# Kernel tuning notes

Hardware: AMD Instinct MI355X
Metric: run time of the kernel (lower is better)

Reference implementation:

```python
import jax, jax.numpy as jnp
import numpy as np

H = 1024
V = 50257
S = 4096


def gru_cell(x, h, W_ih, W_hh, b_ih, b_hh):
    # x: (1, in), h: (1, H). PyTorch gate order: r, z, n
    gi = x @ W_ih.T + b_ih  # (1, 3H)
    gh = h @ W_hh.T + b_hh
    i_r, i_z, i_n = jnp.split(gi, 3, axis=1)
    h_r, h_z, h_n = jnp.split(gh, 3, axis=1)
    r = jax.nn.sigmoid(i_r + h_r)
    z = jax.nn.sigmoid(i_z + h_z)
    n = jnp.tanh(i_n + r * h_n)
    return (1.0 - z) * n + z * h


def setup_inputs() -> dict:
    key = jax.random.key(0)
    ks = jax.random.split(key, 16)
    s = 0.02
    return {
        "word_input": jax.random.randint(ks[0], (1,), 0, V),
        "last_context": jax.random.normal(ks[1], (1, H), jnp.float32),
        "last_hidden": jax.random.normal(ks[2], (2, 1, H), jnp.float32),
        "encoder_outputs": jax.random.normal(ks[3], (S, 1, H), jnp.float32),
        "emb": jax.random.normal(ks[4], (V, H), jnp.float32) * s,
        "W_ih0": jax.random.normal(ks[5], (3 * H, 2 * H), jnp.float32) * s,
        "W_hh0": jax.random.normal(ks[6], (3 * H, H), jnp.float32) * s,
        "b_ih0": jnp.zeros((3 * H,), jnp.float32),
        "b_hh0": jnp.zeros((3 * H,), jnp.float32),
        "W_ih1": jax.random.normal(ks[7], (3 * H, H), jnp.float32) * s,
        "W_hh1": jax.random.normal(ks[8], (3 * H, H), jnp.float32) * s,
        "b_ih1": jnp.zeros((3 * H,), jnp.float32),
        "b_hh1": jnp.zeros((3 * H,), jnp.float32),
        "W_attn": jax.random.normal(ks[9], (H, H), jnp.float32) * s,
        "b_attn": jnp.zeros((H,), jnp.float32),
        "W_out": jax.random.normal(ks[10], (V, 2 * H), jnp.float32) * s,
        "b_out": jnp.zeros((V,), jnp.float32),
    }


def reference(word_input, last_context, last_hidden, encoder_outputs,
              emb, W_ih0, W_hh0, b_ih0, b_hh0, W_ih1, W_hh1, b_ih1, b_hh1,
              W_attn, b_attn, W_out, b_out):
    # embedding lookup -> (1, H); rnn input (1, 2H)
    word_embedded = emb[word_input].reshape(1, H)
    rnn_in = jnp.concatenate([word_embedded, last_context], axis=1)
    # 2-layer GRU, single timestep (dropout inactive at eval)
    h0 = gru_cell(rnn_in, last_hidden[0], W_ih0, W_hh0, b_ih0, b_hh0)
    h1 = gru_cell(h0, last_hidden[1], W_ih1, W_hh1, b_ih1, b_hh1)
    rnn_output = h1  # (1, H)
    hidden = jnp.stack([h0, h1], axis=0)  # (2, 1, H)
    # Bahdanau-style attention, batched (replaces per-timestep Python loop)
    enc = encoder_outputs[:, 0, :]  # (S, H)
    energies = (enc @ W_attn.T + b_attn) @ rnn_output[0]  # (S,)
    attn = jax.nn.softmax(energies)  # (S,)
    attn_weights = attn.reshape(1, 1, S)
    context = (attn[None, :] @ enc)  # (1, H)
    # output projection + log-softmax over vocab
    logits = jnp.concatenate([rnn_output, context], axis=1) @ W_out.T + b_out
    output = jax.nn.log_softmax(logits, axis=1)  # (1, V)
    return output, context, hidden, attn_weights
```

## Files before the change

### kernel.cpp

```cpp
#include <hip/hip_runtime.h>
#include <math.h>

constexpr int kH  = 1024;
constexpr int kV  = 50257;
constexpr int kS  = 4096;
constexpr int kH4 = kH / 4;
constexpr int kH2 = 2 * kH;

constexpr int WS_H0     = 0;
constexpr int WS_GH1    = 1024;
constexpr int WS_H1     = 4096;
constexpr int WS_V      = 5120;
constexpr int WS_CTX    = 6144;
constexpr int WS_ATTN   = 7168;
constexpr int WS_E      = 11264;
constexpr int WS_SC     = 15360;
constexpr int WS_PM     = 15424;
constexpr int WS_PS     = 15488;
constexpr int WS_LOGITS = 15552;

constexpr int OUT_LOGITS = 0;
constexpr int OUT_CTX    = kV;
constexpr int OUT_HID    = kV + kH;
constexpr int OUT_ATTN   = kV + kH + 2 * kH;

__device__ __forceinline__ float wred_sum(float v) {
#pragma unroll
  for (int o = 32; o > 0; o >>= 1) v += __shfl_down(v, o, 64);
  return v;
}
__device__ __forceinline__ float wred_max(float v) {
#pragma unroll
  for (int o = 32; o > 0; o >>= 1) v = fmaxf(v, __shfl_down(v, o, 64));
  return v;
}
__device__ __forceinline__ float sigmoidf_(float x) { return 1.0f / (1.0f + __expf(-x)); }
__device__ __forceinline__ float dot4(float4 a, float4 b) {
  return a.x * b.x + a.y * b.y + a.z * b.z + a.w * b.w;
}

__global__ void k1_gru0_gh1(const int* __restrict__ wi_p, const float* __restrict__ lc,
                            const float* __restrict__ lh, const float* __restrict__ emb,
                            const float* __restrict__ W_ih0, const float* __restrict__ W_hh0,
                            const float* __restrict__ b_ih0, const float* __restrict__ b_hh0,
                            const float* __restrict__ W_hh1, const float* __restrict__ b_hh1,
                            float* __restrict__ ws) {
  const int wave = threadIdx.x >> 6, lane = threadIdx.x & 63;
  const int b = blockIdx.x;
  if (b < 256) {
    const int j = b * 4 + wave;
    const int wi = wi_p[0];
    const float4* embr = (const float4*)(emb + (size_t)wi * kH);
    const float4* lc4  = (const float4*)lc;
    const float4* Wr = (const float4*)(W_ih0 + (size_t)j * kH2);
    const float4* Wz = (const float4*)(W_ih0 + (size_t)(j + kH) * kH2);
    const float4* Wn = (const float4*)(W_ih0 + (size_t)(j + 2 * kH) * kH2);
    float ar = 0.f, az = 0.f, an = 0.f;
#pragma unroll
    for (int i = 0; i < 8; i++) {
      const int idx = lane + i * 64;
      const float4 xv = (idx < kH4) ? embr[idx] : lc4[idx - kH4];
      ar += dot4(Wr[idx], xv);
      az += dot4(Wz[idx], xv);
      an += dot4(Wn[idx], xv);
    }
    const float4* Ur = (const float4*)(W_hh0 + (size_t)j * kH);
    const float4* Uz = (const float4*)(W_hh0 + (size_t)(j + kH) * kH);
    const float4* Un = (const float4*)(W_hh0 + (size_t)(j + 2 * kH) * kH);
    const float4* h4 = (const float4*)lh;
    float br = 0.f, bz = 0.f, bn = 0.f;
#pragma unroll
    for (int i = 0; i < 4; i++) {
      const int idx = lane + i * 64;
      const float4 hv = h4[idx];
      br += dot4(Ur[idx], hv);
      bz += dot4(Uz[idx], hv);
      bn += dot4(Un[idx], hv);
    }
    ar = wred_sum(ar); az = wred_sum(az); an = wred_sum(an);
    br = wred_sum(br); bz = wred_sum(bz); bn = wred_sum(bn);
    if (lane == 0) {
      const float ir = ar + b_ih0[j],          hr = br + b_hh0[j];
      const float iz = az + b_ih0[j + kH],     hz = bz + b_hh0[j + kH];
      const float in_ = an + b_ih0[j + 2 * kH], hn = bn + b_hh0[j + 2 * kH];
      const float r = sigmoidf_(ir + hr);
      const float z = sigmoidf_(iz + hz);
      const float n = tanhf(in_ + r * hn);
      ws[WS_H0 + j] = (1.f - z) * n + z * lh[j];
    }
  } else {
    const int row = (b - 256) * 4 + wave;
    const float4* W  = (const float4*)(W_hh1 + (size_t)row * kH);
    const float4* h4 = (const float4*)(lh + kH);
    float a = 0.f;
#pragma unroll
    for (int i = 0; i < 4; i++) {
      const int idx = lane + i * 64;
      a += dot4(W[idx], h4[idx]);
    }
    a = wred_sum(a);
    if (lane == 0) ws[WS_GH1 + row] = a + b_hh1[row];
  }
}

__global__ void k2_gru1(const float* __restrict__ lh, const float* __restrict__ W_ih1,
                        const float* __restrict__ b_ih1, float* __restrict__ ws,
                        float* __restrict__ out) {
  const int wave = threadIdx.x >> 6, lane = threadIdx.x & 63;
  const int j = blockIdx.x * 4 + wave;
  const float4* x4 = (const float4*)(ws + WS_H0);
  const float4* Wr = (const float4*)(W_ih1 + (size_t)j * kH);
  const float4* Wz = (const float4*)(W_ih1 + (size_t)(j + kH) * kH);
  const float4* Wn = (const float4*)(W_ih1 + (size_t)(j + 2 * kH) * kH);
  float ar = 0.f, az = 0.f, an = 0.f;
#pragma unroll
  for (int i = 0; i < 4; i++) {
    const int idx = lane + i * 64;
    const float4 xv = x4[idx];
    ar += dot4(Wr[idx], xv);
    az += dot4(Wz[idx], xv);
    an += dot4(Wn[idx], xv);
  }
  ar = wred_sum(ar); az = wred_sum(az); an = wred_sum(an);
  if (lane == 0) {
    const float r = sigmoidf_(ar + b_ih1[j] + ws[WS_GH1 + j]);
    const float z = sigmoidf_(az + b_ih1[j + kH] + ws[WS_GH1 + j + kH]);
    const float n = tanhf(an + b_ih1[j + 2 * kH] + r * ws[WS_GH1 + j + 2 * kH]);
    const float h1 = (1.f - z) * n + z * lh[kH + j];
    ws[WS_H1 + j] = h1;
    out[OUT_HID + kH + j] = h1;
    out[OUT_HID + j] = ws[WS_H0 + j];
  }
  if (blockIdx.x < 4) ws[WS_V + blockIdx.x * 256 + threadIdx.x] = 0.f;
}

__global__ void k3_attnv(const float* __restrict__ W_attn, const float* __restrict__ b_attn,
                         float* __restrict__ ws) {
  __shared__ float red[4];
  const int b = blockIdx.x, t = threadIdx.x;
  const int wave = t >> 6, lane = t & 63;
  if (b < 64) {
    const float4* W4 = (const float4*)W_attn;
    float4 acc = make_float4(0.f, 0.f, 0.f, 0.f);
    const int j0 = b * 16;
#pragma unroll
    for (int jj = 0; jj < 16; jj++) {
      const int j = j0 + jj;
      const float s = ws[WS_H1 + j];
      const float4 w = W4[(size_t)j * kH4 + t];
      acc.x += s * w.x; acc.y += s * w.y; acc.z += s * w.z; acc.w += s * w.w;
    }
    atomicAdd(&ws[WS_V + 4 * t + 0], acc.x);
    atomicAdd(&ws[WS_V + 4 * t + 1], acc.y);
    atomicAdd(&ws[WS_V + 4 * t + 2], acc.z);
    atomicAdd(&ws[WS_V + 4 * t + 3], acc.w);
  } else {
    float a = 0.f;
    for (int i = t; i < kH; i += 256) a += b_attn[i] * ws[WS_H1 + i];
    const float wsum = wred_sum(a);
    if (lane == 0) red[wave] = wsum;
    __syncthreads();
    if (t == 0) ws[WS_SC + 0] = red[0] + red[1] + red[2] + red[3];
  }
}

__global__ void k4_energies(const float* __restrict__ enc, float* __restrict__ ws) {
  const int wave = threadIdx.x >> 6, lane = threadIdx.x & 63;
  const int s = blockIdx.x * 4 + wave;
  const float4* e4 = (const float4*)(enc + (size_t)s * kH);
  const float4* v4 = (const float4*)(ws + WS_V);
  float a = 0.f;
#pragma unroll
  for (int i = 0; i < 4; i++) {
    const int idx = lane + i * 64;
    a += dot4(e4[idx], v4[idx]);
  }
  a = wred_sum(a);
  if (lane == 0) ws[WS_E + s] = a + ws[WS_SC + 0];
}

__global__ void k5_softmax(float* __restrict__ ws, float* __restrict__ out) {
  __shared__ float red[16];
  const int t = threadIdx.x, lane = t & 63, wave = t >> 6;
  const float4 e = ((const float4*)(ws + WS_E))[t];
  float m = fmaxf(fmaxf(e.x, e.y), fmaxf(e.z, e.w));
  float wm = wred_max(m);
  if (lane == 0) red[wave] = wm;
  __syncthreads();
  if (wave == 0) {
    float x = (lane < 16) ? red[lane] : -INFINITY;
    x = wred_max(x);
    if (lane == 0) red[0] = x;
  }
  __syncthreads();
  m = red[0];
  __syncthreads();
  float4 ex;
  ex.x = __expf(e.x - m); ex.y = __expf(e.y - m);
  ex.z = __expf(e.z - m); ex.w = __expf(e.w - m);
  float s = ex.x + ex.y + ex.z + ex.w;
  float wsum = wred_sum(s);
  if (lane == 0) red[wave] = wsum;
  __syncthreads();
  if (wave == 0) {
    float x = (lane < 16) ? red[lane] : 0.f;
    x = wred_sum(x);
    if (lane == 0) red[0] = x;
  }
  __syncthreads();
  const float inv = 1.0f / red[0];
  float4 a4 = make_float4(ex.x * inv, ex.y * inv, ex.z * inv, ex.w * inv);
  ((float4*)(ws + WS_ATTN))[t] = a4;
  out[OUT_ATTN + 4 * t + 0] = a4.x;
  out[OUT_ATTN + 4 * t + 1] = a4.y;
  out[OUT_ATTN + 4 * t + 2] = a4.z;
  out[OUT_ATTN + 4 * t + 3] = a4.w;
  ws[WS_CTX + t] = 0.f;
}

__global__ void k6_context(const float* __restrict__ enc, float* __restrict__ ws) {
  const int b = blockIdx.x, t = threadIdx.x;
  const float4* e4 = (const float4*)enc;
  float4 acc = make_float4(0.f, 0.f, 0.f, 0.f);
  const int s0 = b * 64;
  for (int ss = 0; ss < 64; ss++) {
    const int s = s0 + ss;
    const float a = ws[WS_ATTN + s];
    const float4 ev = e4[(size_t)s * kH4 + t];
    acc.x += a * ev.x; acc.y += a * ev.y; acc.z += a * ev.z; acc.w += a * ev.w;
  }
  atomicAdd(&ws[WS_CTX + 4 * t + 0], acc.x);
  atomicAdd(&ws[WS_CTX + 4 * t + 1], acc.y);
  atomicAdd(&ws[WS_CTX + 4 * t + 2], acc.z);
  atomicAdd(&ws[WS_CTX + 4 * t + 3], acc.w);
}

__global__ void k7_logits(const float* __restrict__ W_out, const float* __restrict__ b_out,
                          float* __restrict__ ws) {
  const int wave = threadIdx.x >> 6, lane = threadIdx.x & 63;
  const int row = blockIdx.x * 4 + wave;
  if (row >= kV) return;
  const float4* W4 = (const float4*)(W_out + (size_t)row * kH2);
  const float4* h14 = (const float4*)(ws + WS_H1);
  const float4* c4  = (const float4*)(ws + WS_CTX);
  float a = 0.f;
#pragma unroll
  for (int i = 0; i < 8; i++) {
    const int idx = lane + i * 64;
    const float4 xv = (idx < kH4) ? h14[idx] : c4[idx - kH4];
    a += dot4(W4[idx], xv);
  }
  a = wred_sum(a);
  if (lane == 0) ws[WS_LOGITS + row] = a + b_out[row];
}

__global__ void k8a_partial(float* __restrict__ ws) {
  __shared__ float red[4];
  const int b = blockIdx.x, t = threadIdx.x;
  const int wave = t >> 6, lane = t & 63;
  const int g0 = b * 256 + t;
  float vals[4];
  int nv = 0;
  float m = -INFINITY;
  for (int g = g0; g < kV; g += 64 * 256) {
    const float x = ws[WS_LOGITS + g];
    vals[nv++] = x;
    m = fmaxf(m, x);
  }
  float wm = wred_max(m);
  if (lane == 0) red[wave] = wm;
  __syncthreads();
  const float bm = fmaxf(fmaxf(red[0], red[1]), fmaxf(red[2], red[3]));
  float s = 0.f;
  for (int i = 0; i < nv; i++) s += __expf(vals[i] - bm);
  float wsum = wred_sum(s);
  __syncthreads();
  if (lane == 0) red[wave] = wsum;
  __syncthreads();
  if (t == 0) {
    ws[WS_PM + b] = bm;
    ws[WS_PS + b] = red[0] + red[1] + red[2] + red[3];
  }
}

__global__ void k8b_combine(float* __restrict__ ws) {
  const int lane = threadIdx.x;
  const float m = ws[WS_PM + lane];
  float gm = wred_max(m);
  gm = __shfl(gm, 0, 64);
  const float s = ws[WS_PS + lane] * __expf(m - gm);
  const float gs = wred_sum(s);
  if (lane == 0) {
    ws[WS_SC + 1] = gm;
    ws[WS_SC + 2] = logf(gs);
  }
}

__global__ void k8c_output(const float* __restrict__ ws, float* __restrict__ out) {
  const int g = blockIdx.x * 256 + threadIdx.x;
  const float shift = ws[WS_SC + 1] + ws[WS_SC + 2];
  if (g < kV) out[OUT_LOGITS + g] = ws[WS_LOGITS + g] - shift;
  if (g < kH) out[OUT_CTX + g] = ws[WS_CTX + g];
}

extern "C" void kernel_launch(void* const* d_in, const int* in_sizes, int n_in,
                              void* d_out, int out_size, void* d_ws, size_t ws_size,
                              hipStream_t stream) {
  const int*   wi     = (const int*)d_in[0];
  const float* lc     = (const float*)d_in[1];
  const float* lh     = (const float*)d_in[2];
  const float* enc    = (const float*)d_in[3];
  const float* emb    = (const float*)d_in[4];
  const float* W_ih0  = (const float*)d_in[5];
  const float* W_hh0  = (const float*)d_in[6];
  const float* b_ih0  = (const float*)d_in[7];
  const float* b_hh0  = (const float*)d_in[8];
  const float* W_ih1  = (const float*)d_in[9];
  const float* W_hh1  = (const float*)d_in[10];
  const float* b_ih1  = (const float*)d_in[11];
  const float* b_hh1  = (const float*)d_in[12];
  const float* W_attn = (const float*)d_in[13];
  const float* b_attn = (const float*)d_in[14];
  const float* W_out  = (const float*)d_in[15];
  const float* b_out  = (const float*)d_in[16];
  float* out = (float*)d_out;
  float* ws  = (float*)d_ws;

  k1_gru0_gh1<<<1024, 256, 0, stream>>>(wi, lc, lh, emb, W_ih0, W_hh0, b_ih0, b_hh0,
                                        W_hh1, b_hh1, ws);
  k2_gru1<<<256, 256, 0, stream>>>(lh, W_ih1, b_ih1, ws, out);
  k3_attnv<<<65, 256, 0, stream>>>(W_attn, b_attn, ws);
  k4_energies<<<1024, 256, 0, stream>>>(enc, ws);
  k5_softmax<<<1, 1024, 0, stream>>>(ws, out);
  k6_context<<<64, 256, 0, stream>>>(enc, ws);
  k7_logits<<<(kV + 3) / 4, 256, 0, stream>>>(W_out, b_out, ws);
  k8a_partial<<<64, 256, 0, stream>>>(ws);
  k8b_combine<<<1, 64, 0, stream>>>(ws);
  k8c_output<<<(kV + 255) / 256, 256, 0, stream>>>(ws, out);
}
```

Measured before the change: 708.2 us.

## Split output projection across stages, use nontemporal weight loads, merge LSE kernels

The vocab projection is split in two. The h1 half of W_out is now computed inside the attention-vector kernel as soon as h1 is ready, and the context half is added later once the context is known. All streamed weight loads become nontemporal, to avoid polluting the cache with single-use data. The two-stage max/log-sum-exp reduction is replaced by one 1024-thread block, which removes a launch but serialises a pass over 50K logits.

```diff
diff --git a/kernel.cpp b/kernel.cpp
--- a/kernel.cpp
+++ b/kernel.cpp
@@ -15,9 +15,7 @@
 constexpr int WS_ATTN   = 7168;
 constexpr int WS_E      = 11264;
 constexpr int WS_SC     = 15360;
-constexpr int WS_PM     = 15424;
-constexpr int WS_PS     = 15488;
-constexpr int WS_LOGITS = 15552;
+constexpr int WS_LOGITS = 15424;
 
 constexpr int OUT_LOGITS = 0;
 constexpr int OUT_CTX    = kV;
@@ -37,6 +35,12 @@
 __device__ __forceinline__ float sigmoidf_(float x) { return 1.0f / (1.0f + __expf(-x)); }
 __device__ __forceinline__ float dot4(float4 a, float4 b) {
   return a.x * b.x + a.y * b.y + a.z * b.z + a.w * b.w;
+}
+
+typedef float f32x4_t __attribute__((ext_vector_type(4)));
+__device__ __forceinline__ float4 ntld(const float4* p) {
+  f32x4_t v = __builtin_nontemporal_load((const f32x4_t*)p);
+  return make_float4(v.x, v.y, v.z, v.w);
 }
 
 __global__ void k1_gru0_gh1(const int* __restrict__ wi_p, const float* __restrict__ lc,
@@ -60,9 +64,9 @@
     for (int i = 0; i < 8; i++) {
       const int idx = lane + i * 64;
       const float4 xv = (idx < kH4) ? embr[idx] : lc4[idx - kH4];
-      ar += dot4(Wr[idx], xv);
-      az += dot4(Wz[idx], xv);
-      an += dot4(Wn[idx], xv);
+      ar += dot4(ntld(Wr + idx), xv);
+      az += dot4(ntld(Wz + idx), xv);
+      an += dot4(ntld(Wn + idx), xv);
     }
     const float4* Ur = (const float4*)(W_hh0 + (size_t)j * kH);
     const float4* Uz = (const float4*)(W_hh0 + (size_t)(j + kH) * kH);
@@ -73,9 +77,9 @@
     for (int i = 0; i < 4; i++) {
       const int idx = lane + i * 64;
       const float4 hv = h4[idx];
-      br += dot4(Ur[idx], hv);
-      bz += dot4(Uz[idx], hv);
-      bn += dot4(Un[idx], hv);
+      br += dot4(ntld(Ur + idx), hv);
+      bz += dot4(ntld(Uz + idx), hv);
+      bn += dot4(ntld(Un + idx), hv);
     }
     ar = wred_sum(ar); az = wred_sum(az); an = wred_sum(an);
     br = wred_sum(br); bz = wred_sum(bz); bn = wred_sum(bn);
@@ -96,7 +100,7 @@
 #pragma unroll
     for (int i = 0; i < 4; i++) {
       const int idx = lane + i * 64;
-      a += dot4(W[idx], h4[idx]);
+      a += dot4(ntld(W + idx), h4[idx]);
     }
     a = wred_sum(a);
     if (lane == 0) ws[WS_GH1 + row] = a + b_hh1[row];
@@ -117,9 +121,9 @@
   for (int i = 0; i < 4; i++) {
     const int idx = lane + i * 64;
     const float4 xv = x4[idx];
-    ar += dot4(Wr[idx], xv);
-    az += dot4(Wz[idx], xv);
-    an += dot4(Wn[idx], xv);
+    ar += dot4(ntld(Wr + idx), xv);
+    az += dot4(ntld(Wz + idx), xv);
+    an += dot4(ntld(Wn + idx), xv);
   }
   ar = wred_sum(ar); az = wred_sum(az); an = wred_sum(an);
   if (lane == 0) {
@@ -134,11 +138,27 @@
   if (blockIdx.x < 4) ws[WS_V + blockIdx.x * 256 + threadIdx.x] = 0.f;
 }
 
-__global__ void k3_attnv(const float* __restrict__ W_attn, const float* __restrict__ b_attn,
-                         float* __restrict__ ws) {
+__global__ void k3_attnv_logh1(const float* __restrict__ W_attn, const float* __restrict__ b_attn,
+                               const float* __restrict__ W_out, const float* __restrict__ b_out,
+                               float* __restrict__ ws) {
   __shared__ float red[4];
   const int b = blockIdx.x, t = threadIdx.x;
   const int wave = t >> 6, lane = t & 63;
+  if (b >= 65) {
+    const int row = (b - 65) * 4 + wave;
+    if (row >= kV) return;
+    const float4* W4  = (const float4*)(W_out + (size_t)row * kH2);
+    const float4* h14 = (const float4*)(ws + WS_H1);
+    float a = 0.f;
+#pragma unroll
+    for (int i = 0; i < 4; i++) {
+      const int idx = lane + i * 64;
+      a += dot4(ntld(W4 + idx), h14[idx]);
+    }
+    a = wred_sum(a);
+    if (lane == 0) ws[WS_LOGITS + row] = a + b_out[row];
+    return;
+  }
   if (b < 64) {
     const float4* W4 = (const float4*)W_attn;
     float4 acc = make_float4(0.f, 0.f, 0.f, 0.f);
@@ -147,7 +167,7 @@
     for (int jj = 0; jj < 16; jj++) {
       const int j = j0 + jj;
       const float s = ws[WS_H1 + j];
-      const float4 w = W4[(size_t)j * kH4 + t];
+      const float4 w = ntld(W4 + (size_t)j * kH4 + t);
       acc.x += s * w.x; acc.y += s * w.y; acc.z += s * w.z; acc.w += s * w.w;
     }
     atomicAdd(&ws[WS_V + 4 * t + 0], acc.x);
@@ -235,62 +255,47 @@
   atomicAdd(&ws[WS_CTX + 4 * t + 3], acc.w);
 }
 
-__global__ void k7_logits(const float* __restrict__ W_out, const float* __restrict__ b_out,
-                          float* __restrict__ ws) {
+__global__ void k7_logits_ctx(const float* __restrict__ W_out, float* __restrict__ ws) {
   const int wave = threadIdx.x >> 6, lane = threadIdx.x & 63;
   const int row = blockIdx.x * 4 + wave;
   if (row >= kV) return;
-  const float4* W4 = (const float4*)(W_out + (size_t)row * kH2);
-  const float4* h14 = (const float4*)(ws + WS_H1);
-  const float4* c4  = (const float4*)(ws + WS_CTX);
+  const float4* W4 = (const float4*)(W_out + (size_t)row * kH2 + kH);
+  const float4* c4 = (const float4*)(ws + WS_CTX);
   float a = 0.f;
 #pragma unroll
-  for (int i = 0; i < 8; i++) {
+  for (int i = 0; i < 4; i++) {
     const int idx = lane + i * 64;
-    const float4 xv = (idx < kH4) ? h14[idx] : c4[idx - kH4];
-    a += dot4(W4[idx], xv);
+    a += dot4(ntld(W4 + idx), c4[idx]);
   }
   a = wred_sum(a);
-  if (lane == 0) ws[WS_LOGITS + row] = a + b_out[row];
-}
-
-__global__ void k8a_partial(float* __restrict__ ws) {
-  __shared__ float red[4];
-  const int b = blockIdx.x, t = threadIdx.x;
-  const int wave = t >> 6, lane = t & 63;
-  const int g0 = b * 256 + t;
-  float vals[4];
-  int nv = 0;
+  if (lane == 0) ws[WS_LOGITS + row] += a;
+}
+
+__global__ void k8m_maxlse(float* __restrict__ ws) {
+  __shared__ float red[16];
+  const int t = threadIdx.x, lane = t & 63, wave = t >> 6;
   float m = -INFINITY;
-  for (int g = g0; g < kV; g += 64 * 256) {
-    const float x = ws[WS_LOGITS + g];
-    vals[nv++] = x;
-    m = fmaxf(m, x);
-  }
-  float wm = wred_max(m);
-  if (lane == 0) red[wave] = wm;
-  __syncthreads();
-  const float bm = fmaxf(fmaxf(red[0], red[1]), fmaxf(red[2], red[3]));
+  for (int g = t; g < kV; g += 1024) m = fmaxf(m, ws[WS_LOGITS + g]);
+  m = wred_max(m);
+  if (lane == 0) red[wave] = m;
+  __syncthreads();
+  if (wave == 0) {
+    float x = (lane < 16) ? red[lane] : -INFINITY;
+    x = wred_max(x);
+    if (lane == 0) red[0] = x;
+  }
+  __syncthreads();
+  const float gm = red[0];
+  __syncthreads();
   float s = 0.f;
-  for (int i = 0; i < nv; i++) s += __expf(vals[i] - bm);
-  float wsum = wred_sum(s);
-  __syncthreads();
-  if (lane == 0) red[wave] = wsum;
+  for (int g = t; g < kV; g += 1024) s += __expf(ws[WS_LOGITS + g] - gm);
+  s = wred_sum(s);
+  if (lane == 0) red[wave] = s;
   __syncthreads();
   if (t == 0) {
-    ws[WS_PM + b] = bm;
-    ws[WS_PS + b] = red[0] + red[1] + red[2] + red[3];
-  }
-}
-
-__global__ void k8b_combine(float* __restrict__ ws) {
-  const int lane = threadIdx.x;
-  const float m = ws[WS_PM + lane];
-  float gm = wred_max(m);
-  gm = __shfl(gm, 0, 64);
-  const float s = ws[WS_PS + lane] * __expf(m - gm);
-  const float gs = wred_sum(s);
-  if (lane == 0) {
+    float gs = 0.f;
+#pragma unroll
+    for (int i = 0; i < 16; i++) gs += red[i];
     ws[WS_SC + 1] = gm;
     ws[WS_SC + 2] = logf(gs);
   }
@@ -326,15 +331,16 @@
   float* out = (float*)d_out;
   float* ws  = (float*)d_ws;
 
+  constexpr int kLogitBlocks = (kV + 3) / 4;
+
   k1_gru0_gh1<<<1024, 256, 0, stream>>>(wi, lc, lh, emb, W_ih0, W_hh0, b_ih0, b_hh0,
                                         W_hh1, b_hh1, ws);
   k2_gru1<<<256, 256, 0, stream>>>(lh, W_ih1, b_ih1, ws, out);
-  k3_attnv<<<65, 256, 0, stream>>>(W_attn, b_attn, ws);
+  k3_attnv_logh1<<<65 + kLogitBlocks, 256, 0, stream>>>(W_attn, b_attn, W_out, b_out, ws);
   k4_energies<<<1024, 256, 0, stream>>>(enc, ws);
   k5_softmax<<<1, 1024, 0, stream>>>(ws, out);
   k6_context<<<64, 256, 0, stream>>>(enc, ws);
-  k7_logits<<<(kV + 3) / 4, 256, 0, stream>>>(W_out, b_out, ws);
-  k8a_partial<<<64, 256, 0, stream>>>(ws);
-  k8b_combine<<<1, 64, 0, stream>>>(ws);
+  k7_logits_ctx<<<kLogitBlocks, 256, 0, stream>>>(W_out, ws);
+  k8m_maxlse<<<1, 1024, 0, stream>>>(ws);
   k8c_output<<<(kV + 255) / 256, 256, 0, stream>>>(ws, out);
 }
```

New measurement: 694.1 us. 2.0% less time.
